# Performance work log

Measured on AMD Instinct MI355X. Metric: run time of the kernel, lower is better.

The kernel has to match this reference:

```python
import jax, jax.numpy as jnp
import numpy as np

N, DIM, G, K = 100000, 512, 4, 16
GD = DIM // G
EPS = 1e-5

def _ln(x, g, b):
    mu = jnp.mean(x, axis=-1, keepdims=True)
    var = jnp.mean((x - mu) ** 2, axis=-1, keepdims=True)
    return (x - mu) / jnp.sqrt(var + EPS) * g + b

def setup_inputs() -> dict:
    key = jax.random.key(0)
    ks = jax.random.split(key, 12)
    s = 1.0 / np.sqrt(GD)
    return {
        "features": jax.random.normal(ks[0], (N, DIM), jnp.float32),
        "coords": jax.random.uniform(ks[1], (N, 3), jnp.float32),
        "neighbors": jax.random.randint(ks[2], (N, K), 0, N),
        "Wq": jax.random.normal(ks[3], (G, GD, GD), jnp.float32) * s,
        "Wk": jax.random.normal(ks[4], (G, GD, GD), jnp.float32) * s,
        "Wv": jax.random.normal(ks[5], (G, GD, GD), jnp.float32) * s,
        "Wo": jax.random.normal(ks[6], (DIM, DIM), jnp.float32) / np.sqrt(DIM),
        "bo": jnp.zeros((DIM,), jnp.float32),
        "ln1_g": jnp.ones((DIM,), jnp.float32),
        "ln1_b": jnp.zeros((DIM,), jnp.float32),
        "ln2_g": jnp.ones((DIM,), jnp.float32),
        "ln2_b": jnp.zeros((DIM,), jnp.float32),
        "W1": jax.random.normal(ks[7], (2 * DIM, DIM), jnp.float32) / np.sqrt(DIM),
        "b1": jnp.zeros((2 * DIM,), jnp.float32),
        "W2": jax.random.normal(ks[8], (DIM, 2 * DIM), jnp.float32) / np.sqrt(2 * DIM),
        "b2": jnp.zeros((DIM,), jnp.float32),
    }

def reference(features, coords, neighbors, Wq, Wk, Wv, Wo, bo, ln1_g, ln1_b, ln2_g, ln2_b, W1, b1, W2, b2):
    n = features.shape[0]
    residual = features
    x = _ln(features, ln1_g, ln1_b)
    xg = x.reshape(n, G, GD)                      # chunk along feature dim == group reshape
    # per-group Linear (no bias): y = x @ W.T with W (out,in)
    q = jnp.einsum('ngd,god->ngo', xg, Wq)
    k = jnp.einsum('ngd,god->ngo', xg, Wk)
    v = jnp.einsum('ngd,god->ngo', xg, Wv)
    nk = k[neighbors]                             # (N,K,G,GD) gather
    nv = v[neighbors]
    scale = jnp.asarray(1.0 / np.sqrt(GD), x.dtype)
    scores = jnp.einsum('ngd,nkgd->nkg', q, nk) * scale
    w = jax.nn.softmax(scores, axis=1)
    attn = jnp.einsum('nkg,nkgd->ngd', w, nv).reshape(n, DIM)
    out = attn @ Wo.T + bo + residual
    res2 = out
    y = _ln(out, ln2_g, ln2_b)
    y = jax.nn.gelu(y @ W1.T + b1, approximate=False) @ W2.T + b2
    return y + res2
```

## Files before the change

kernel.cpp:

```cpp
#include <hip/hip_runtime.h>
#include <hip/hip_bf16.h>
#include <math.h>

#define NPTS 100000
#define PAD_ROWS 100096
#define DIM 512
#define GRP 4
#define GD 128
#define K_NBR 16
#define EPS 1e-5f

using bf16x8 = __attribute__((ext_vector_type(8))) short;
using f32x4  = __attribute__((ext_vector_type(4))) float;
using short4v = __attribute__((ext_vector_type(4))) short;

__device__ inline float bf2f(short s) {
    unsigned u = ((unsigned)(unsigned short)s) << 16;
    union { unsigned u; float f; } c; c.u = u; return c.f;
}
__device__ inline short f2bf(float f) {
    union { float f; unsigned u; } c; c.f = f;
    unsigned u = c.u;
    unsigned r = (u + 0x7fffu + ((u >> 16) & 1u)) >> 16;
    return (short)r;
}

__device__ __forceinline__ void gload_lds16(short* lds, const short* g) {
    __builtin_amdgcn_global_load_lds(
        (const __attribute__((address_space(1))) unsigned int*)g,
        (__attribute__((address_space(3))) unsigned int*)lds, 16, 0, 0);
}

__global__ void cvt_kernel(const float* __restrict__ src, short* __restrict__ dst, int n) {
    int i = blockIdx.x * blockDim.x + threadIdx.x;
    int stride = gridDim.x * blockDim.x;
    for (; i < n; i += stride) dst[i] = f2bf(src[i]);
}

__global__ void prep_m_kernel(const float* __restrict__ wq, const float* __restrict__ wk,
                              short* __restrict__ mt) {
    int ge = blockIdx.x;
    int g = ge >> 7, e = ge & 127;
    int d = threadIdx.x;
    const float* Wq = wq + (size_t)g * GD * GD;
    const float* Wk = wk + (size_t)g * GD * GD;
    float acc = 0.0f;
    for (int o = 0; o < GD; ++o)
        acc += Wq[(size_t)o * GD + d] * Wk[(size_t)o * GD + e];
    mt[(size_t)ge * GD + d] = f2bf(acc * 0.08838834764831845f);
}

__global__ void prep_wov_kernel(const float* __restrict__ wo, const float* __restrict__ wv,
                                short* __restrict__ wov) {
    int o = blockIdx.x;
    int i = threadIdx.x;
    int g = i >> 7, i0 = i & 127;
    float acc = 0.0f;
    for (int d = 0; d < GD; ++d)
        acc += wo[(size_t)o * DIM + g * GD + d] * wv[((size_t)g * GD + d) * GD + i0];
    wov[(size_t)o * DIM + i] = f2bf(acc);
}

__global__ void ln_kernel(const float* __restrict__ in, const float* __restrict__ g,
                          const float* __restrict__ b, short* __restrict__ out) {
    int row = blockIdx.x;
    int tid = threadIdx.x;
    if (row >= NPTS) {
        short4v z; z[0] = 0; z[1] = 0; z[2] = 0; z[3] = 0;
        *(short4v*)(out + (size_t)row * DIM + tid * 4) = z;
        return;
    }
    const float4 x = *(const float4*)(in + (size_t)row * DIM + tid * 4);
    float s  = x.x + x.y + x.z + x.w;
    float sq = x.x * x.x + x.y * x.y + x.z * x.z + x.w * x.w;
    for (int m = 1; m < 64; m <<= 1) {
        s  += __shfl_xor(s, m);
        sq += __shfl_xor(sq, m);
    }
    __shared__ float ss[2], ssq[2];
    int wv = tid >> 6;
    if ((tid & 63) == 0) { ss[wv] = s; ssq[wv] = sq; }
    __syncthreads();
    s = ss[0] + ss[1]; sq = ssq[0] + ssq[1];
    float mu = s * (1.0f / DIM);
    float var = sq * (1.0f / DIM) - mu * mu;
    float rstd = rsqrtf(var + EPS);
    const float4 gg = *(const float4*)(g + tid * 4);
    const float4 bb = *(const float4*)(b + tid * 4);
    short4v o;
    o[0] = f2bf((x.x - mu) * rstd * gg.x + bb.x);
    o[1] = f2bf((x.y - mu) * rstd * gg.y + bb.y);
    o[2] = f2bf((x.z - mu) * rstd * gg.z + bb.z);
    o[3] = f2bf((x.w - mu) * rstd * gg.w + bb.w);
    *(short4v*)(out + (size_t)row * DIM + tid * 4) = o;
}

__global__ void ln_bf16_kernel(const short* __restrict__ in, const float* __restrict__ g,
                               const float* __restrict__ b, short* __restrict__ out) {
    int row = blockIdx.x;
    int tid = threadIdx.x;
    if (row >= NPTS) {
        short4v z; z[0] = 0; z[1] = 0; z[2] = 0; z[3] = 0;
        *(short4v*)(out + (size_t)row * DIM + tid * 4) = z;
        return;
    }
    short4v xi = *(const short4v*)(in + (size_t)row * DIM + tid * 4);
    float x0 = bf2f(xi[0]), x1 = bf2f(xi[1]), x2 = bf2f(xi[2]), x3 = bf2f(xi[3]);
    float s  = x0 + x1 + x2 + x3;
    float sq = x0 * x0 + x1 * x1 + x2 * x2 + x3 * x3;
    for (int m = 1; m < 64; m <<= 1) {
        s  += __shfl_xor(s, m);
        sq += __shfl_xor(sq, m);
    }
    __shared__ float ss[2], ssq[2];
    int wv = tid >> 6;
    if ((tid & 63) == 0) { ss[wv] = s; ssq[wv] = sq; }
    __syncthreads();
    s = ss[0] + ss[1]; sq = ssq[0] + ssq[1];
    float mu = s * (1.0f / DIM);
    float var = sq * (1.0f / DIM) - mu * mu;
    float rstd = rsqrtf(var + EPS);
    const float4 gg = *(const float4*)(g + tid * 4);
    const float4 bb = *(const float4*)(b + tid * 4);
    short4v o;
    o[0] = f2bf((x0 - mu) * rstd * gg.x + bb.x);
    o[1] = f2bf((x1 - mu) * rstd * gg.y + bb.y);
    o[2] = f2bf((x2 - mu) * rstd * gg.z + bb.z);
    o[3] = f2bf((x3 - mu) * rstd * gg.w + bb.w);
    *(short4v*)(out + (size_t)row * DIM + tid * 4) = o;
}

__device__ __forceinline__ void stage_tile(short* As, short* Bs,
        const short* aS, int as_, const short* bS, int bs_, int tid) {
    int ldRow = tid >> 2;
    int ldCol = (tid & 3) * 8;
    gload_lds16(As + (ldRow)      * 32 + ldCol, aS + (size_t)(ldRow)      * as_ + ldCol);
    gload_lds16(As + (ldRow + 64) * 32 + ldCol, aS + (size_t)(ldRow + 64) * as_ + ldCol);
    gload_lds16(Bs + (ldRow)      * 32 + ldCol, bS + (size_t)(ldRow)      * bs_ + ldCol);
    gload_lds16(Bs + (ldRow + 64) * 32 + ldCol, bS + (size_t)(ldRow + 64) * bs_ + ldCol);
}

__device__ __forceinline__ void compute_tile(const short* As, const short* Bs,
        int wr, int wc, int r, int ks, f32x4 (&acc)[4][4]) {
    bf16x8 a[4];
    #pragma unroll
    for (int m = 0; m < 4; ++m)
        a[m] = *(const bf16x8*)(As + (wr * 64 + m * 16 + r) * 32 + ks * 8);
    #pragma unroll
    for (int n = 0; n < 4; ++n) {
        bf16x8 b = *(const bf16x8*)(Bs + (wc * 64 + n * 16 + r) * 32 + ks * 8);
        #pragma unroll
        for (int m = 0; m < 4; ++m)
            acc[m][n] = __builtin_amdgcn_mfma_f32_16x16x32_bf16(a[m], b, acc[m][n], 0, 0, 0);
    }
}

template<int NK>
__device__ __forceinline__ void gemm_tile(
        const short* __restrict__ aBase, int as_,
        const short* __restrict__ bBase, int bs_,
        short* As0, short* Bs0, short* As1, short* Bs1, f32x4 (&acc)[4][4]) {
    int tid = threadIdx.x;
    int lane = tid & 63, wave = tid >> 6;
    int wr = wave >> 1, wc = wave & 1;
    int r = lane & 15, ks = lane >> 4;
    stage_tile(As0, Bs0, aBase, as_, bBase, bs_, tid);
    __syncthreads();
    #pragma unroll
    for (int kt = 0; kt < NK; kt += 2) {
        if (kt + 1 < NK)
            stage_tile(As1, Bs1, aBase + (kt + 1) * 32, as_, bBase + (kt + 1) * 32, bs_, tid);
        compute_tile(As0, Bs0, wr, wc, r, ks, acc);
        __syncthreads();
        if (kt + 2 < NK)
            stage_tile(As0, Bs0, aBase + (kt + 2) * 32, as_, bBase + (kt + 2) * 32, bs_, tid);
        compute_tile(As1, Bs1, wr, wc, r, ks, acc);
        __syncthreads();
    }
}

#define GEMM_LDS \
    __shared__ short As0[128 * 32], Bs0[128 * 32], As1[128 * 32], Bs1[128 * 32]

__global__ __launch_bounds__(256) void qproj_kernel(
        const short* __restrict__ x, const short* __restrict__ mt,
        short* __restrict__ qp) {
    GEMM_LDS;
    int nwg = gridDim.x;
    int bid = blockIdx.x;
    int tile = (bid & 7) * (nwg >> 3) + (bid >> 3);
    int rb = tile >> 2, g = tile & 3;
    int rowbase = rb * 128;
    int tid = threadIdx.x;
    int lane = tid & 63, wave = tid >> 6;
    int wr = wave >> 1, wc = wave & 1;
    int r = lane & 15, ks = lane >> 4;
    f32x4 acc[4][4];
    #pragma unroll
    for (int m = 0; m < 4; ++m)
        #pragma unroll
        for (int n = 0; n < 4; ++n)
            #pragma unroll
            for (int e = 0; e < 4; ++e) acc[m][n][e] = 0.0f;
    gemm_tile<4>(x + (size_t)rowbase * DIM + g * GD, DIM,
                 mt + (size_t)g * GD * GD, GD, As0, Bs0, As1, Bs1, acc);
    #pragma unroll
    for (int m = 0; m < 4; ++m)
        #pragma unroll
        for (int n = 0; n < 4; ++n)
            #pragma unroll
            for (int rr = 0; rr < 4; ++rr) {
                int orow = rowbase + wr * 64 + m * 16 + ks * 4 + rr;
                int lcol = wc * 64 + n * 16 + r;
                qp[(size_t)orow * DIM + g * GD + lcol] = f2bf(acc[m][n][rr]);
            }
}

__global__ __launch_bounds__(256) void attn_kernel(
        const short* __restrict__ qp, const short* __restrict__ x,
        const int* __restrict__ nbrs, short* __restrict__ t_out) {
    int b = blockIdx.x;
    int xcd = b & 7;
    int g = xcd >> 1;
    int quad = (b >> 3) * 2 + (xcd & 1);
    int tid = threadIdx.x;
    int wv = tid >> 6, lane = tid & 63;
    int n = quad * 4 + wv;
    int s = lane >> 4, t = lane & 15;
    int4 nbj = *(const int4*)(nbrs + (size_t)n * K_NBR + s * 4);
    int nbarr[4] = {nbj.x, nbj.y, nbj.z, nbj.w};
    size_t goff = (size_t)g * GD + t * 8;
    size_t qbase = (size_t)n * DIM + goff;
    bf16x8 qf = *(const bf16x8*)(qp + qbase);
    float qv[8];
    #pragma unroll
    for (int e = 0; e < 8; ++e) qv[e] = bf2f(qf[e]);
    bf16x8 xf[4];
    #pragma unroll
    for (int p = 0; p < 4; ++p)
        xf[p] = *(const bf16x8*)(x + (size_t)nbarr[p] * DIM + goff);
    float sc[4];
    #pragma unroll
    for (int p = 0; p < 4; ++p) {
        float dd = 0.0f;
        #pragma unroll
        for (int e = 0; e < 8; ++e) dd += qv[e] * bf2f(xf[p][e]);
        dd += __shfl_xor(dd, 1);
        dd += __shfl_xor(dd, 2);
        dd += __shfl_xor(dd, 4);
        dd += __shfl_xor(dd, 8);
        sc[p] = dd;
    }
    float mx = fmaxf(fmaxf(sc[0], sc[1]), fmaxf(sc[2], sc[3]));
    mx = fmaxf(mx, __shfl_xor(mx, 16));
    mx = fmaxf(mx, __shfl_xor(mx, 32));
    float ew[4]; float ssum = 0.0f;
    #pragma unroll
    for (int p = 0; p < 4; ++p) { ew[p] = __expf(sc[p] - mx); ssum += ew[p]; }
    ssum += __shfl_xor(ssum, 16);
    ssum += __shfl_xor(ssum, 32);
    float acc[8];
    #pragma unroll
    for (int d0 = 0; d0 < 8; ++d0) acc[d0] = 0.0f;
    #pragma unroll
    for (int p = 0; p < 4; ++p) {
        #pragma unroll
        for (int d0 = 0; d0 < 8; ++d0) acc[d0] += ew[p] * bf2f(xf[p][d0]);
    }
    #pragma unroll
    for (int d0 = 0; d0 < 8; ++d0) {
        acc[d0] += __shfl_xor(acc[d0], 16);
        acc[d0] += __shfl_xor(acc[d0], 32);
    }
    if (s == 0) {
        float inv = 1.0f / ssum;
        bf16x8 o;
        #pragma unroll
        for (int d0 = 0; d0 < 8; ++d0) o[d0] = f2bf(acc[d0] * inv);
        *(bf16x8*)(t_out + qbase) = o;
    }
}

__global__ __launch_bounds__(256) void outproj_kernel(
        const short* __restrict__ tbuf, const short* __restrict__ wov,
        const float* __restrict__ bo, const float* __restrict__ features,
        short* __restrict__ res2) {
    GEMM_LDS;
    int nwg = gridDim.x;
    int bid = blockIdx.x;
    int tile = (bid & 7) * (nwg >> 3) + (bid >> 3);
    int rb = tile >> 2, cb = tile & 3;
    int rowbase = rb * 128, colbase = cb * 128;
    int tid = threadIdx.x;
    int lane = tid & 63, wave = tid >> 6;
    int wr = wave >> 1, wc = wave & 1;
    int r = lane & 15, ks = lane >> 4;
    f32x4 acc[4][4];
    #pragma unroll
    for (int m = 0; m < 4; ++m)
        #pragma unroll
        for (int n = 0; n < 4; ++n)
            #pragma unroll
            for (int e = 0; e < 4; ++e) acc[m][n][e] = 0.0f;
    gemm_tile<16>(tbuf + (size_t)rowbase * DIM, DIM,
                  wov + (size_t)colbase * DIM, DIM, As0, Bs0, As1, Bs1, acc);
    #pragma unroll
    for (int m = 0; m < 4; ++m)
        #pragma unroll
        for (int n = 0; n < 4; ++n)
            #pragma unroll
            for (int rr = 0; rr < 4; ++rr) {
                int orow = rowbase + wr * 64 + m * 16 + ks * 4 + rr;
                int ocol = colbase + wc * 64 + n * 16 + r;
                if (orow < NPTS) {
                    float val = acc[m][n][rr] + bo[ocol] + features[(size_t)orow * DIM + ocol];
                    res2[(size_t)orow * DIM + ocol] = f2bf(val);
                }
            }
}

__global__ __launch_bounds__(256) void ffn1_kernel(
        const short* __restrict__ y, const short* __restrict__ w1,
        const float* __restrict__ b1, short* __restrict__ h) {
    GEMM_LDS;
    int nwg = gridDim.x;
    int bid = blockIdx.x;
    int tile = (bid & 7) * (nwg >> 3) + (bid >> 3);
    int rb = tile >> 3, cb = tile & 7;
    int rowbase = rb * 128, colbase = cb * 128;
    int tid = threadIdx.x;
    int lane = tid & 63, wave = tid >> 6;
    int wr = wave >> 1, wc = wave & 1;
    int r = lane & 15, ks = lane >> 4;
    f32x4 acc[4][4];
    #pragma unroll
    for (int m = 0; m < 4; ++m)
        #pragma unroll
        for (int n = 0; n < 4; ++n)
            #pragma unroll
            for (int e = 0; e < 4; ++e) acc[m][n][e] = 0.0f;
    gemm_tile<16>(y + (size_t)rowbase * DIM, DIM,
                  w1 + (size_t)colbase * DIM, DIM, As0, Bs0, As1, Bs1, acc);
    #pragma unroll
    for (int m = 0; m < 4; ++m)
        #pragma unroll
        for (int n = 0; n < 4; ++n)
            #pragma unroll
            for (int rr = 0; rr < 4; ++rr) {
                int orow = rowbase + wr * 64 + m * 16 + ks * 4 + rr;
                int ocol = colbase + wc * 64 + n * 16 + r;
                float xv = acc[m][n][rr] + b1[ocol];
                float xc = fminf(fmaxf(xv, -9.0f), 9.0f);
                float u = xc * (0.7978845608028654f + 0.0356774081f * xc * xc);
                float e2 = __expf(2.0f * u);
                float th = (e2 - 1.0f) / (e2 + 1.0f);
                float gl = 0.5f * xv * (1.0f + th);
                h[(size_t)orow * (2 * DIM) + ocol] = f2bf(gl);
            }
}

__global__ __launch_bounds__(256) void ffn2_kernel(
        const short* __restrict__ h, const short* __restrict__ w2,
        const float* __restrict__ b2, const short* __restrict__ res2,
        float* __restrict__ out) {
    GEMM_LDS;
    int nwg = gridDim.x;
    int bid = blockIdx.x;
    int tile = (bid & 7) * (nwg >> 3) + (bid >> 3);
    int rb = tile >> 2, cb = tile & 3;
    int rowbase = rb * 128, colbase = cb * 128;
    int tid = threadIdx.x;
    int lane = tid & 63, wave = tid >> 6;
    int wr = wave >> 1, wc = wave & 1;
    int r = lane & 15, ks = lane >> 4;
    f32x4 acc[4][4];
    #pragma unroll
    for (int m = 0; m < 4; ++m)
        #pragma unroll
        for (int n = 0; n < 4; ++n)
            #pragma unroll
            for (int e = 0; e < 4; ++e) acc[m][n][e] = 0.0f;
    gemm_tile<32>(h + (size_t)rowbase * (2 * DIM), 2 * DIM,
                  w2 + (size_t)colbase * (2 * DIM), 2 * DIM, As0, Bs0, As1, Bs1, acc);
    #pragma unroll
    for (int m = 0; m < 4; ++m)
        #pragma unroll
        for (int n = 0; n < 4; ++n)
            #pragma unroll
            for (int rr = 0; rr < 4; ++rr) {
                int orow = rowbase + wr * 64 + m * 16 + ks * 4 + rr;
                int ocol = colbase + wc * 64 + n * 16 + r;
                if (orow < NPTS) {
                    size_t idx = (size_t)orow * DIM + ocol;
                    out[idx] = acc[m][n][rr] + b2[ocol] + bf2f(res2[idx]);
                }
            }
}

extern "C" void kernel_launch(void* const* d_in, const int* in_sizes, int n_in,
                              void* d_out, int out_size, void* d_ws, size_t ws_size,
                              hipStream_t stream) {
    const float* features = (const float*)d_in[0];
    const int*   neighbors = (const int*)d_in[2];
    const float* Wq = (const float*)d_in[3];
    const float* Wk = (const float*)d_in[4];
    const float* Wv = (const float*)d_in[5];
    const float* Wo = (const float*)d_in[6];
    const float* bo = (const float*)d_in[7];
    const float* ln1_g = (const float*)d_in[8];
    const float* ln1_b = (const float*)d_in[9];
    const float* ln2_g = (const float*)d_in[10];
    const float* ln2_b = (const float*)d_in[11];
    const float* W1 = (const float*)d_in[12];
    const float* b1 = (const float*)d_in[13];
    const float* W2 = (const float*)d_in[14];
    const float* b2 = (const float*)d_in[15];
    float* out = (float*)d_out;

    size_t slotElems = (size_t)PAD_ROWS * DIM;
    short* s0 = (short*)d_ws;
    short* s1 = s0 + slotElems;
    short* s2 = s1 + slotElems;
    short* s3 = s2 + slotElems;
    short* mt_b  = s3 + slotElems;
    short* wov_b = mt_b + GRP * GD * GD;
    short* w1_b  = wov_b + DIM * DIM;
    short* w2_b  = w1_b + 2 * DIM * DIM;

    cvt_kernel<<<256, 256, 0, stream>>>(W1, w1_b, 2 * DIM * DIM);
    cvt_kernel<<<256, 256, 0, stream>>>(W2, w2_b, 2 * DIM * DIM);
    prep_m_kernel<<<GRP * GD, GD, 0, stream>>>(Wq, Wk, mt_b);
    prep_wov_kernel<<<DIM, DIM, 0, stream>>>(Wo, Wv, wov_b);

    ln_kernel<<<PAD_ROWS, 128, 0, stream>>>(features, ln1_g, ln1_b, s0);

    qproj_kernel<<<(PAD_ROWS / 128) * 4, 256, 0, stream>>>(s0, mt_b, s1);

    attn_kernel<<<NPTS, 256, 0, stream>>>(s1, s0, neighbors, s2);

    outproj_kernel<<<(PAD_ROWS / 128) * 4, 256, 0, stream>>>(s2, wov_b, bo, features, s3);

    ln_bf16_kernel<<<PAD_ROWS, 128, 0, stream>>>(s3, ln2_g, ln2_b, s0);

    ffn1_kernel<<<(PAD_ROWS / 128) * 8, 256, 0, stream>>>(s0, w1_b, b1, s1);

    ffn2_kernel<<<(PAD_ROWS / 128) * 4, 256, 0, stream>>>(s1, w2_b, b2, s3, out);
}
```

Before: 1.072 ms.

## Fuse FFN up and down projections keeping hidden activations in LDS

Replaces the separate FFN1 (GEMM+GELU writing h to global) and FFN2 kernels with a single kernel per 64-row block. The GELU output is stored in a padded LDS buffer and consumed directly by the second GEMM, which removes the global round trip of the 100k x 1024 bf16 hidden tensor. Weights are read straight from global memory without LDS staging, and the large LDS footprint (about 130KB) limits occupancy to one block per CU. Each block also recomputes over the full W1 and W2 tiles.

```diff
diff --git a/kernel.cpp b/kernel.cpp
--- a/kernel.cpp
+++ b/kernel.cpp
@@ -9,6 +9,7 @@
 #define GD 128
 #define K_NBR 16
 #define EPS 1e-5f
+#define H_LD 1028
 
 using bf16x8 = __attribute__((ext_vector_type(8))) short;
 using f32x4  = __attribute__((ext_vector_type(4))) float;
@@ -319,80 +320,105 @@
             }
 }
 
-__global__ __launch_bounds__(256) void ffn1_kernel(
+__global__ __launch_bounds__(512) void ffn_fused_kernel(
         const short* __restrict__ y, const short* __restrict__ w1,
-        const float* __restrict__ b1, short* __restrict__ h) {
-    GEMM_LDS;
-    int nwg = gridDim.x;
-    int bid = blockIdx.x;
-    int tile = (bid & 7) * (nwg >> 3) + (bid >> 3);
-    int rb = tile >> 3, cb = tile & 7;
-    int rowbase = rb * 128, colbase = cb * 128;
+        const float* __restrict__ b1, const short* __restrict__ w2,
+        const float* __restrict__ b2, const short* __restrict__ res2,
+        float* __restrict__ out) {
+    __shared__ short hbuf[64 * H_LD];
+    __shared__ short Ab[2][64 * 64];
     int tid = threadIdx.x;
     int lane = tid & 63, wave = tid >> 6;
-    int wr = wave >> 1, wc = wave & 1;
     int r = lane & 15, ks = lane >> 4;
-    f32x4 acc[4][4];
-    #pragma unroll
-    for (int m = 0; m < 4; ++m)
-        #pragma unroll
-        for (int n = 0; n < 4; ++n)
-            #pragma unroll
-            for (int e = 0; e < 4; ++e) acc[m][n][e] = 0.0f;
-    gemm_tile<16>(y + (size_t)rowbase * DIM, DIM,
-                  w1 + (size_t)colbase * DIM, DIM, As0, Bs0, As1, Bs1, acc);
-    #pragma unroll
-    for (int m = 0; m < 4; ++m)
-        #pragma unroll
-        for (int n = 0; n < 4; ++n)
+    int rowbase = blockIdx.x * 64;
+    const short* yR = y + (size_t)rowbase * DIM;
+    int srow = tid >> 3, schunk = tid & 7;
+
+    f32x4 acc1[4][8];
+    #pragma unroll
+    for (int m = 0; m < 4; ++m)
+        #pragma unroll
+        for (int n = 0; n < 8; ++n)
+            #pragma unroll
+            for (int e = 0; e < 4; ++e) acc1[m][n][e] = 0.0f;
+    int colbase1 = wave * 128;
+    gload_lds16(Ab[0] + srow * 64 + schunk * 8,
+                yR + (size_t)srow * DIM + 0 + ((schunk ^ (srow & 7)) * 8));
+    __syncthreads();
+    for (int kt = 0; kt < 8; ++kt) {
+        if (kt + 1 < 8)
+            gload_lds16(Ab[(kt + 1) & 1] + srow * 64 + schunk * 8,
+                        yR + (size_t)srow * DIM + (kt + 1) * 64 + ((schunk ^ (srow & 7)) * 8));
+        const short* A = Ab[kt & 1];
+        #pragma unroll
+        for (int ks2 = 0; ks2 < 2; ++ks2) {
+            int kc8 = ((ks2 * 4 + ks) ^ (r & 7)) * 8;
+            bf16x8 a[4];
+            #pragma unroll
+            for (int m = 0; m < 4; ++m)
+                a[m] = *(const bf16x8*)(A + (m * 16 + r) * 64 + kc8);
+            int kg = kt * 64 + ks2 * 32 + ks * 8;
+            #pragma unroll
+            for (int n = 0; n < 8; ++n) {
+                bf16x8 b = *(const bf16x8*)(w1 + (size_t)(colbase1 + n * 16 + r) * DIM + kg);
+                #pragma unroll
+                for (int m = 0; m < 4; ++m)
+                    acc1[m][n] = __builtin_amdgcn_mfma_f32_16x16x32_bf16(a[m], b, acc1[m][n], 0, 0, 0);
+            }
+        }
+        __syncthreads();
+    }
+    #pragma unroll
+    for (int m = 0; m < 4; ++m)
+        #pragma unroll
+        for (int n = 0; n < 8; ++n) {
+            int hcol = colbase1 + n * 16 + r;
+            float bb = b1[hcol];
             #pragma unroll
             for (int rr = 0; rr < 4; ++rr) {
-                int orow = rowbase + wr * 64 + m * 16 + ks * 4 + rr;
-                int ocol = colbase + wc * 64 + n * 16 + r;
-                float xv = acc[m][n][rr] + b1[ocol];
+                int hrow = m * 16 + ks * 4 + rr;
+                float xv = acc1[m][n][rr] + bb;
                 float xc = fminf(fmaxf(xv, -9.0f), 9.0f);
                 float u = xc * (0.7978845608028654f + 0.0356774081f * xc * xc);
                 float e2 = __expf(2.0f * u);
                 float th = (e2 - 1.0f) / (e2 + 1.0f);
-                float gl = 0.5f * xv * (1.0f + th);
-                h[(size_t)orow * (2 * DIM) + ocol] = f2bf(gl);
+                hbuf[hrow * H_LD + hcol] = f2bf(0.5f * xv * (1.0f + th));
             }
-}
-
-__global__ __launch_bounds__(256) void ffn2_kernel(
-        const short* __restrict__ h, const short* __restrict__ w2,
-        const float* __restrict__ b2, const short* __restrict__ res2,
-        float* __restrict__ out) {
-    GEMM_LDS;
-    int nwg = gridDim.x;
-    int bid = blockIdx.x;
-    int tile = (bid & 7) * (nwg >> 3) + (bid >> 3);
-    int rb = tile >> 2, cb = tile & 3;
-    int rowbase = rb * 128, colbase = cb * 128;
-    int tid = threadIdx.x;
-    int lane = tid & 63, wave = tid >> 6;
-    int wr = wave >> 1, wc = wave & 1;
-    int r = lane & 15, ks = lane >> 4;
-    f32x4 acc[4][4];
-    #pragma unroll
-    for (int m = 0; m < 4; ++m)
-        #pragma unroll
-        for (int n = 0; n < 4; ++n)
-            #pragma unroll
-            for (int e = 0; e < 4; ++e) acc[m][n][e] = 0.0f;
-    gemm_tile<32>(h + (size_t)rowbase * (2 * DIM), 2 * DIM,
-                  w2 + (size_t)colbase * (2 * DIM), 2 * DIM, As0, Bs0, As1, Bs1, acc);
+        }
+    __syncthreads();
+
+    f32x4 acc2[4][4];
+    #pragma unroll
+    for (int m = 0; m < 4; ++m)
+        #pragma unroll
+        for (int n = 0; n < 4; ++n)
+            #pragma unroll
+            for (int e = 0; e < 4; ++e) acc2[m][n][e] = 0.0f;
+    int colbase2 = wave * 64;
+    for (int k2 = 0; k2 < 1024; k2 += 32) {
+        bf16x8 a[4];
+        #pragma unroll
+        for (int m = 0; m < 4; ++m)
+            a[m] = *(const bf16x8*)(hbuf + (m * 16 + r) * H_LD + k2 + ks * 8);
+        #pragma unroll
+        for (int n = 0; n < 4; ++n) {
+            bf16x8 b = *(const bf16x8*)(w2 + (size_t)(colbase2 + n * 16 + r) * 1024 + k2 + ks * 8);
+            #pragma unroll
+            for (int m = 0; m < 4; ++m)
+                acc2[m][n] = __builtin_amdgcn_mfma_f32_16x16x32_bf16(a[m], b, acc2[m][n], 0, 0, 0);
+        }
+    }
     #pragma unroll
     for (int m = 0; m < 4; ++m)
         #pragma unroll
         for (int n = 0; n < 4; ++n)
             #pragma unroll
             for (int rr = 0; rr < 4; ++rr) {
-                int orow = rowbase + wr * 64 + m * 16 + ks * 4 + rr;
-                int ocol = colbase + wc * 64 + n * 16 + r;
+                int orow = rowbase + m * 16 + ks * 4 + rr;
+                int ocol = colbase2 + n * 16 + r;
                 if (orow < NPTS) {
                     size_t idx = (size_t)orow * DIM + ocol;
-                    out[idx] = acc[m][n][rr] + b2[ocol] + bf2f(res2[idx]);
+                    out[idx] = acc2[m][n][rr] + b2[ocol] + bf2f(res2[idx]);
                 }
             }
 }
@@ -442,7 +468,5 @@
 
     ln_bf16_kernel<<<PAD_ROWS, 128, 0, stream>>>(s3, ln2_g, ln2_b, s0);
 
-    ffn1_kernel<<<(PAD_ROWS / 128) * 8, 256, 0, stream>>>(s0, w1_b, b1, s1);
-
-    ffn2_kernel<<<(PAD_ROWS / 128) * 4, 256, 0, stream>>>(s1, w2_b, b2, s3, out);
-}
+    ffn_fused_kernel<<<PAD_ROWS / 64, 512, 0, stream>>>(s0, w1_b, b1, w2_b, b2, s3, out);
+}
```

Measured after the change: 1.316 ms. 1.23x slower.

## Split FFN into row segments so hidden activations stay cache-resident

Applied to the files above, without the earlier changes.

Runs the FFN1/FFN2 pair over four row segments, reusing the same hidden buffer, so each segment's bf16 hidden activations can stay in the last-level cache between the two GEMMs instead of round-tripping through HBM. Adds more kernel launches and per-segment tail inefficiency, and serializes segments on the stream.

```diff
diff --git a/kernel.cpp b/kernel.cpp
--- a/kernel.cpp
+++ b/kernel.cpp
@@ -320,8 +320,8 @@
 }
 
 __global__ __launch_bounds__(256) void ffn1_kernel(
-        const short* __restrict__ y, const short* __restrict__ w1,
-        const float* __restrict__ b1, short* __restrict__ h) {
+        const short* __restrict__ ySeg, const short* __restrict__ w1,
+        const float* __restrict__ b1, short* __restrict__ hSeg) {
     GEMM_LDS;
     int nwg = gridDim.x;
     int bid = blockIdx.x;
@@ -339,7 +339,7 @@
         for (int n = 0; n < 4; ++n)
             #pragma unroll
             for (int e = 0; e < 4; ++e) acc[m][n][e] = 0.0f;
-    gemm_tile<16>(y + (size_t)rowbase * DIM, DIM,
+    gemm_tile<16>(ySeg + (size_t)rowbase * DIM, DIM,
                   w1 + (size_t)colbase * DIM, DIM, As0, Bs0, As1, Bs1, acc);
     #pragma unroll
     for (int m = 0; m < 4; ++m)
@@ -355,14 +355,14 @@
                 float e2 = __expf(2.0f * u);
                 float th = (e2 - 1.0f) / (e2 + 1.0f);
                 float gl = 0.5f * xv * (1.0f + th);
-                h[(size_t)orow * (2 * DIM) + ocol] = f2bf(gl);
+                hSeg[(size_t)orow * (2 * DIM) + ocol] = f2bf(gl);
             }
 }
 
 __global__ __launch_bounds__(256) void ffn2_kernel(
-        const short* __restrict__ h, const short* __restrict__ w2,
-        const float* __restrict__ b2, const short* __restrict__ res2,
-        float* __restrict__ out) {
+        const short* __restrict__ hSeg, const short* __restrict__ w2,
+        const float* __restrict__ b2, const short* __restrict__ res2Seg,
+        float* __restrict__ outSeg, int rowsLeft) {
     GEMM_LDS;
     int nwg = gridDim.x;
     int bid = blockIdx.x;
@@ -380,7 +380,7 @@
         for (int n = 0; n < 4; ++n)
             #pragma unroll
             for (int e = 0; e < 4; ++e) acc[m][n][e] = 0.0f;
-    gemm_tile<32>(h + (size_t)rowbase * (2 * DIM), 2 * DIM,
+    gemm_tile<32>(hSeg + (size_t)rowbase * (2 * DIM), 2 * DIM,
                   w2 + (size_t)colbase * (2 * DIM), 2 * DIM, As0, Bs0, As1, Bs1, acc);
     #pragma unroll
     for (int m = 0; m < 4; ++m)
@@ -390,9 +390,9 @@
             for (int rr = 0; rr < 4; ++rr) {
                 int orow = rowbase + wr * 64 + m * 16 + ks * 4 + rr;
                 int ocol = colbase + wc * 64 + n * 16 + r;
-                if (orow < NPTS) {
+                if (orow < rowsLeft) {
                     size_t idx = (size_t)orow * DIM + ocol;
-                    out[idx] = acc[m][n][rr] + b2[ocol] + bf2f(res2[idx]);
+                    outSeg[idx] = acc[m][n][rr] + b2[ocol] + bf2f(res2Seg[idx]);
                 }
             }
 }
@@ -442,7 +442,19 @@
 
     ln_bf16_kernel<<<PAD_ROWS, 128, 0, stream>>>(s3, ln2_g, ln2_b, s0);
 
-    ffn1_kernel<<<(PAD_ROWS / 128) * 8, 256, 0, stream>>>(s0, w1_b, b1, s1);
-
-    ffn2_kernel<<<(PAD_ROWS / 128) * 4, 256, 0, stream>>>(s1, w2_b, b2, s3, out);
-}
+    {
+        const int segTiles[4] = {196, 196, 196, 194};
+        int tileOff = 0;
+        for (int sgi = 0; sgi < 4; ++sgi) {
+            int nt = segTiles[sgi];
+            size_t ro = (size_t)tileOff * 128;
+            const short* ySeg   = s0 + ro * DIM;
+            const short* res2Sg = s3 + ro * DIM;
+            float*       outSeg = out + ro * DIM;
+            int rowsLeft = NPTS - (int)ro;
+            ffn1_kernel<<<nt * 8, 256, 0, stream>>>(ySeg, w1_b, b1, s1);
+            ffn2_kernel<<<nt * 4, 256, 0, stream>>>(s1, w2_b, b2, res2Sg, outSeg, rowsLeft);
+            tileOff += nt;
+        }
+    }
+}
```

After: 1.166 ms. 8.7% more time.

## Use triple-buffered LDS pipeline with vmcnt waits for big GEMMs

Applied to the files above, without the earlier changes.

Replaces the double-buffered GEMM main loop in the out-projection and both FFN kernels with a three-stage LDS ring. Global loads are issued two tiles ahead, and explicit s_waitcnt vmcnt counts plus raw s_barrier calls replace __syncthreads. The aim is to hide global load latency behind MFMA compute. In exchange it uses 1.5x the LDS, which may reduce occupancy, and correctness depends on stage_tile issuing exactly four vector loads per tile.

```diff
diff --git a/kernel.cpp b/kernel.cpp
--- a/kernel.cpp
+++ b/kernel.cpp
@@ -179,13 +179,44 @@
     }
 }
 
-#define GEMM_LDS \
-    __shared__ short As0[128 * 32], Bs0[128 * 32], As1[128 * 32], Bs1[128 * 32]
+#define PB3 (128 * 32)
+template<int NT>
+__device__ __forceinline__ void gemmP3(
+        const short* __restrict__ aBase, int as_,
+        const short* __restrict__ bBase, int bs_,
+        short* P, f32x4 (&acc)[4][4]) {
+    int tid = threadIdx.x;
+    int lane = tid & 63, wave = tid >> 6;
+    int wr = wave >> 1, wc = wave & 1;
+    int r = lane & 15, ks = lane >> 4;
+    stage_tile(P,           P + PB3,           aBase,      as_, bBase,      bs_, tid);
+    stage_tile(P + 2 * PB3, P + 3 * PB3,       aBase + 32, as_, bBase + 32, bs_, tid);
+    #pragma unroll
+    for (int t = 0; t < NT; ++t) {
+        int bn = (t + 2) % 3, bc = t % 3;
+        if (t + 2 < NT) {
+            stage_tile(P + bn * 2 * PB3, P + bn * 2 * PB3 + PB3,
+                       aBase + (size_t)(t + 2) * 32, as_,
+                       bBase + (size_t)(t + 2) * 32, bs_, tid);
+            asm volatile("s_waitcnt vmcnt(8)" ::: "memory");
+        } else if (t + 1 < NT) {
+            asm volatile("s_waitcnt vmcnt(4)" ::: "memory");
+        } else {
+            asm volatile("s_waitcnt vmcnt(0)" ::: "memory");
+        }
+        __builtin_amdgcn_s_barrier();
+        __builtin_amdgcn_sched_barrier(0);
+        compute_tile(P + bc * 2 * PB3, P + bc * 2 * PB3 + PB3, wr, wc, r, ks, acc);
+        __builtin_amdgcn_s_barrier();
+    }
+}
+
+#define GEMMP3_LDS __shared__ short P[6 * PB3]
 
 __global__ __launch_bounds__(256) void qproj_kernel(
         const short* __restrict__ x, const short* __restrict__ mt,
         short* __restrict__ qp) {
-    GEMM_LDS;
+    __shared__ short As0[128 * 32], Bs0[128 * 32], As1[128 * 32], Bs1[128 * 32];
     int nwg = gridDim.x;
     int bid = blockIdx.x;
     int tile = (bid & 7) * (nwg >> 3) + (bid >> 3);
@@ -285,7 +316,7 @@
         const short* __restrict__ tbuf, const short* __restrict__ wov,
         const float* __restrict__ bo, const float* __restrict__ features,
         short* __restrict__ res2) {
-    GEMM_LDS;
+    GEMMP3_LDS;
     int nwg = gridDim.x;
     int bid = blockIdx.x;
     int tile = (bid & 7) * (nwg >> 3) + (bid >> 3);
@@ -302,8 +333,8 @@
         for (int n = 0; n < 4; ++n)
             #pragma unroll
             for (int e = 0; e < 4; ++e) acc[m][n][e] = 0.0f;
-    gemm_tile<16>(tbuf + (size_t)rowbase * DIM, DIM,
-                  wov + (size_t)colbase * DIM, DIM, As0, Bs0, As1, Bs1, acc);
+    gemmP3<16>(tbuf + (size_t)rowbase * DIM, DIM,
+               wov + (size_t)colbase * DIM, DIM, P, acc);
     #pragma unroll
     for (int m = 0; m < 4; ++m)
         #pragma unroll
@@ -322,7 +353,7 @@
 __global__ __launch_bounds__(256) void ffn1_kernel(
         const short* __restrict__ y, const short* __restrict__ w1,
         const float* __restrict__ b1, short* __restrict__ h) {
-    GEMM_LDS;
+    GEMMP3_LDS;
     int nwg = gridDim.x;
     int bid = blockIdx.x;
     int tile = (bid & 7) * (nwg >> 3) + (bid >> 3);
@@ -339,8 +370,8 @@
         for (int n = 0; n < 4; ++n)
             #pragma unroll
             for (int e = 0; e < 4; ++e) acc[m][n][e] = 0.0f;
-    gemm_tile<16>(y + (size_t)rowbase * DIM, DIM,
-                  w1 + (size_t)colbase * DIM, DIM, As0, Bs0, As1, Bs1, acc);
+    gemmP3<16>(y + (size_t)rowbase * DIM, DIM,
+               w1 + (size_t)colbase * DIM, DIM, P, acc);
     #pragma unroll
     for (int m = 0; m < 4; ++m)
         #pragma unroll
@@ -363,7 +394,7 @@
         const short* __restrict__ h, const short* __restrict__ w2,
         const float* __restrict__ b2, const short* __restrict__ res2,
         float* __restrict__ out) {
-    GEMM_LDS;
+    GEMMP3_LDS;
     int nwg = gridDim.x;
     int bid = blockIdx.x;
     int tile = (bid & 7) * (nwg >> 3) + (bid >> 3);
@@ -380,8 +411,8 @@
         for (int n = 0; n < 4; ++n)
             #pragma unroll
             for (int e = 0; e < 4; ++e) acc[m][n][e] = 0.0f;
-    gemm_tile<32>(h + (size_t)rowbase * (2 * DIM), 2 * DIM,
-                  w2 + (size_t)colbase * (2 * DIM), 2 * DIM, As0, Bs0, As1, Bs1, acc);
+    gemmP3<32>(h + (size_t)rowbase * (2 * DIM), 2 * DIM,
+               w2 + (size_t)colbase * (2 * DIM), 2 * DIM, P, acc);
     #pragma unroll
     for (int m = 0; m < 4; ++m)
         #pragma unroll
```

Result: no change. 1.075 ms (+0.2%).
